# Kernel optimization log

Measured on AMD Instinct MI355X. Metric: run time of the kernel, lower is better.

Reference implementation:

```python
import jax, jax.numpy as jnp
import numpy as np

N_NODES = 50000

def gcn_conv(x, src, dst, W, b, n_nodes):
    # PyG GCNConv: add self-loops, symmetric deg^{-1/2} normalization,
    # linear transform, scatter-add aggregation (source -> target), bias.
    loop = jnp.arange(n_nodes, dtype=src.dtype)
    src2 = jnp.concatenate([src, loop])
    dst2 = jnp.concatenate([dst, loop])
    deg = jax.ops.segment_sum(jnp.ones_like(dst2, dtype=x.dtype), dst2, num_segments=n_nodes)
    dinv = jnp.where(deg > 0, jax.lax.rsqrt(deg), 0.0)
    norm = dinv[src2] * dinv[dst2]  # [E + N]
    h = x @ W                        # [N, out]
    msg = h[src2] * norm[:, None]    # gather + scale
    out = jax.ops.segment_sum(msg, dst2, num_segments=n_nodes)
    return out + b

def setup_inputs() -> dict:
    key = jax.random.key(0)
    k1, k2, k3, k4 = jax.random.split(key, 4)
    x = jax.random.normal(k1, (N_NODES, 64), dtype=jnp.float32)
    edge_index = jax.random.randint(k2, (2, 800000), 0, N_NODES, dtype=jnp.int64)
    # Glorot-ish init for weights
    W1 = jax.random.normal(k3, (64, 128), dtype=jnp.float32) * (1.0 / np.sqrt(64))
    b1 = jnp.zeros((128,), dtype=jnp.float32)
    W2 = jax.random.normal(k4, (128, 8), dtype=jnp.float32) * (1.0 / np.sqrt(128))
    b2 = jnp.zeros((8,), dtype=jnp.float32)
    return {"x": x, "edge_index": edge_index, "W1": W1, "b1": b1, "W2": W2, "b2": b2}

def reference(x, edge_index, W1, b1, W2, b2):
    src, dst = edge_index[0], edge_index[1]
    h = gcn_conv(x, src, dst, W1, b1, N_NODES)
    h = jax.nn.relu(h)
    out = gcn_conv(h, src, dst, W2, b2, N_NODES)
    return out
```

## Files before the change

### kernel.cpp

```cpp
#include <hip/hip_runtime.h>

#define IN1 64
#define MID 128
#define OUT2 8
#define YPAD 136
#define CAP 64

__device__ __forceinline__ unsigned short f2bf(float f) {
    unsigned int u = __float_as_uint(f);
    unsigned int r = (u + 0x7fff + ((u >> 16) & 1)) >> 16;
    return (unsigned short)r;
}
__device__ __forceinline__ float bflo(unsigned int u) { return __uint_as_float(u << 16); }
__device__ __forceinline__ float bfhi(unsigned int u) { return __uint_as_float(u & 0xffff0000u); }

__global__ __launch_bounds__(256) void k_fillp(const int* __restrict__ src,
                                               const int* __restrict__ dst,
                                               int* __restrict__ cnt,
                                               unsigned short* __restrict__ col,
                                               int E4, int E, int npx, int slices) {
    int xcd = blockIdx.x & 7;
    int slice = blockIdx.x >> 3;
    int lo = xcd * npx, hi = lo + npx;
    int eps = (E4 + slices - 1) / slices;
    int g0 = slice * eps, g1 = min(E4, g0 + eps);
    for (int g = g0 + (int)threadIdx.x; g < g1; g += 256) {
        int4 sv = ((const int4*)src)[g];
        int4 dv = ((const int4*)dst)[g];
        if (dv.x >= lo && dv.x < hi) {
            int p = atomicAdd(&cnt[dv.x], 1);
            if (p < CAP) col[dv.x * CAP + p] = (unsigned short)sv.x;
        }
        if (dv.y >= lo && dv.y < hi) {
            int p = atomicAdd(&cnt[dv.y], 1);
            if (p < CAP) col[dv.y * CAP + p] = (unsigned short)sv.y;
        }
        if (dv.z >= lo && dv.z < hi) {
            int p = atomicAdd(&cnt[dv.z], 1);
            if (p < CAP) col[dv.z * CAP + p] = (unsigned short)sv.z;
        }
        if (dv.w >= lo && dv.w < hi) {
            int p = atomicAdd(&cnt[dv.w], 1);
            if (p < CAP) col[dv.w * CAP + p] = (unsigned short)sv.w;
        }
    }
    if (blockIdx.x == 0 && threadIdx.x == 0) {
        for (int e = E4 * 4; e < E; ++e) {
            int d = dst[e];
            int p = atomicAdd(&cnt[d], 1);
            if (p < CAP) col[d * CAP + p] = (unsigned short)src[e];
        }
    }
}

__global__ void k_prescale(const float4* __restrict__ x4, const int* __restrict__ cnt,
                           float* __restrict__ dinv, ushort4* __restrict__ xb4, int n16) {
    int gid = blockIdx.x * blockDim.x + threadIdx.x;
    if (gid >= n16) return;
    int row = gid >> 4;
    float d = rsqrtf((float)(cnt[row] + 1));
    if ((gid & 15) == 0) dinv[row] = d;
    float4 vx = x4[gid];
    ushort4 p;
    p.x = f2bf(vx.x * d); p.y = f2bf(vx.y * d);
    p.z = f2bf(vx.z * d); p.w = f2bf(vx.w * d);
    xb4[gid] = p;
}

__global__ __launch_bounds__(256) void k_node(const uint2* __restrict__ xb2,
                                              const int* __restrict__ cnt,
                                              const unsigned short* __restrict__ col,
                                              const float* __restrict__ dinv,
                                              const float* __restrict__ W1,
                                              const float* __restrict__ b1,
                                              const float* __restrict__ W2,
                                              float* __restrict__ z, int n) {
    __shared__ float w2s[MID * OUT2];
    __shared__ float tS[4][4][IN1];
    __shared__ float yS[4][4][YPAD];

    int t = threadIdx.x;
    ((float4*)w2s)[t] = ((const float4*)W2)[t];

    int lane = t & 63, wave = t >> 6;
    int g = lane >> 4;
    int fl2 = lane & 15;
    int q4 = fl2 & 3;
    int row0 = blockIdx.x * 16 + wave * 4;
    int row = row0 + g;
    bool valid = row < n;

    float a0 = 0.f, a1 = 0.f, a2 = 0.f, a3 = 0.f;
    int deg = 0, base = 0;
    if (valid) {
        deg = min(cnt[row], CAP);
        base = row * CAP;
        uint2 u = xb2[(size_t)row * 16 + fl2];
        a0 = bflo(u.x); a1 = bfhi(u.x); a2 = bflo(u.y); a3 = bfhi(u.y);
    }
    int j = 0;
    for (; j + 4 <= deg; j += 4) {
        int cv = col[base + j + q4];
#pragma unroll
        for (int p = 0; p < 4; ++p) {
            int s = __shfl(cv, (g << 4) + p, 64);
            uint2 u = xb2[(size_t)s * 16 + fl2];
            a0 += bflo(u.x); a1 += bfhi(u.x);
            a2 += bflo(u.y); a3 += bfhi(u.y);
        }
    }
    int rem = deg - j;
    if (rem > 0) {
        int cv = col[base + min(j + q4, CAP - 1)];
#pragma unroll
        for (int p = 0; p < 4; ++p) {
            int s = __shfl(cv, (g << 4) + p, 64);
            if (p < rem) {
                uint2 u = xb2[(size_t)s * 16 + fl2];
                a0 += bflo(u.x); a1 += bfhi(u.x);
                a2 += bflo(u.y); a3 += bfhi(u.y);
            }
        }
    }
    {
        float4 w = {a0, a1, a2, a3};
        *(float4*)&tS[wave][g][4 * fl2] = w;
    }

    float dnd[4];
#pragma unroll
    for (int k = 0; k < 4; ++k) dnd[k] = dinv[min(row0 + k, n - 1)];

    float ya0 = 0.f, yb0 = 0.f, ya1 = 0.f, yb1 = 0.f;
    float ya2 = 0.f, yb2 = 0.f, ya3 = 0.f, yb3 = 0.f;
#pragma unroll 4
    for (int k4 = 0; k4 < IN1; k4 += 4) {
        float4 t0 = *(const float4*)&tS[wave][0][k4];
        float4 t1 = *(const float4*)&tS[wave][1][k4];
        float4 t2 = *(const float4*)&tS[wave][2][k4];
        float4 t3 = *(const float4*)&tS[wave][3][k4];
#pragma unroll
        for (int kk = 0; kk < 4; ++kk) {
            int k = k4 + kk;
            float wa = W1[k * MID + lane];
            float wb = W1[k * MID + lane + 64];
            float e0 = (&t0.x)[kk], e1 = (&t1.x)[kk], e2 = (&t2.x)[kk], e3 = (&t3.x)[kk];
            ya0 = fmaf(e0, wa, ya0); yb0 = fmaf(e0, wb, yb0);
            ya1 = fmaf(e1, wa, ya1); yb1 = fmaf(e1, wb, yb1);
            ya2 = fmaf(e2, wa, ya2); yb2 = fmaf(e2, wb, yb2);
            ya3 = fmaf(e3, wa, ya3); yb3 = fmaf(e3, wb, yb3);
        }
    }
    float bl = b1[lane], bh = b1[lane + 64];
    yS[wave][0][lane] = fmaxf(fmaf(ya0, dnd[0], bl), 0.f);
    yS[wave][0][lane + 64] = fmaxf(fmaf(yb0, dnd[0], bh), 0.f);
    yS[wave][1][lane] = fmaxf(fmaf(ya1, dnd[1], bl), 0.f);
    yS[wave][1][lane + 64] = fmaxf(fmaf(yb1, dnd[1], bh), 0.f);
    yS[wave][2][lane] = fmaxf(fmaf(ya2, dnd[2], bl), 0.f);
    yS[wave][2][lane + 64] = fmaxf(fmaf(yb2, dnd[2], bh), 0.f);
    yS[wave][3][lane] = fmaxf(fmaf(ya3, dnd[3], bl), 0.f);
    yS[wave][3][lane + 64] = fmaxf(fmaf(yb3, dnd[3], bh), 0.f);

    __syncthreads();

    int nd2 = lane >> 4, ch = lane & 15;
    float p[OUT2];
#pragma unroll
    for (int c = 0; c < OUT2; ++c) p[c] = 0.0f;
#pragma unroll
    for (int kk = 0; kk < 8; ++kk) {
        int k = kk * 16 + ch;
        float yk = yS[wave][nd2][k];
        float4 wlo = *(const float4*)&w2s[k * OUT2];
        float4 whi = *(const float4*)&w2s[k * OUT2 + 4];
        p[0] = fmaf(yk, wlo.x, p[0]); p[1] = fmaf(yk, wlo.y, p[1]);
        p[2] = fmaf(yk, wlo.z, p[2]); p[3] = fmaf(yk, wlo.w, p[3]);
        p[4] = fmaf(yk, whi.x, p[4]); p[5] = fmaf(yk, whi.y, p[5]);
        p[6] = fmaf(yk, whi.z, p[6]); p[7] = fmaf(yk, whi.w, p[7]);
    }
#pragma unroll
    for (int off = 1; off < 16; off <<= 1) {
#pragma unroll
        for (int c = 0; c < OUT2; ++c) p[c] += __shfl_xor(p[c], off, 64);
    }
    int rw = row0 + nd2;
    if (rw < n && ch < OUT2) {
        z[(size_t)rw * OUT2 + ch] = p[ch] * dinv[rw];
    }
}

__global__ __launch_bounds__(256) void k_gather2(const int* __restrict__ cnt,
                                                 const unsigned short* __restrict__ col,
                                                 const float* __restrict__ z,
                                                 const float* __restrict__ dinv,
                                                 const float* __restrict__ b2,
                                                 float* __restrict__ out, int n) {
    int t = threadIdx.x, lane = t & 63, wave = t >> 6;
    int node = blockIdx.x * 4 + wave;
    if (node >= n) return;
    int nb = lane >> 3, c = lane & 7;
    float acc = (nb == 0) ? z[(size_t)node * OUT2 + c] : 0.0f;
    int deg = min(cnt[node], CAP);
    int base = node * CAP;
    int j = nb;
    for (; j + 8 < deg; j += 16) {
        int s0 = col[base + j], s1 = col[base + j + 8];
        float a0 = z[(size_t)s0 * OUT2 + c];
        float a1 = z[(size_t)s1 * OUT2 + c];
        acc += a0 + a1;
    }
    if (j < deg) acc += z[(size_t)col[base + j] * OUT2 + c];
#pragma unroll
    for (int off = 8; off < 64; off <<= 1) acc += __shfl_xor(acc, off, 64);
    if (lane < OUT2) out[(size_t)node * OUT2 + lane] = fmaf(acc, dinv[node], b2[lane]);
}

extern "C" void kernel_launch(void* const* d_in, const int* in_sizes, int n_in,
                              void* d_out, int out_size, void* d_ws, size_t ws_size,
                              hipStream_t stream) {
    const float* x  = (const float*)d_in[0];
    const int*   ei = (const int*)d_in[1];
    const float* W1 = (const float*)d_in[2];
    const float* b1 = (const float*)d_in[3];
    const float* W2 = (const float*)d_in[4];
    const float* b2 = (const float*)d_in[5];
    float* out = (float*)d_out;

    int N = in_sizes[0] / IN1;
    int E = in_sizes[1] / 2;
    const int* src = ei;
    const int* dst = ei + E;

    int* cnt = (int*)d_ws;
    unsigned short* col = (unsigned short*)(cnt + N);
    float* dinv = (float*)(col + (size_t)N * CAP);
    float* z = dinv + N;
    unsigned short* xb = (unsigned short*)(z + (size_t)N * OUT2);

    const int B = 256;
    int E4 = E / 4;
    int npx = (N + 7) / 8;
    int slices = 192;

    hipMemsetAsync(cnt, 0, (size_t)N * sizeof(int), stream);
    k_fillp<<<slices * 8, B, 0, stream>>>(src, dst, cnt, col, E4, E, npx, slices);
    k_prescale<<<((size_t)N * 16 + B - 1) / B, B, 0, stream>>>((const float4*)x, cnt, dinv,
                                                               (ushort4*)xb, N * 16);
    k_node<<<(N + 15) / 16, 256, 0, stream>>>((const uint2*)xb, cnt, col, dinv, W1, b1, W2, z, N);
    k_gather2<<<(N + 3) / 4, 256, 0, stream>>>(cnt, col, z, dinv, b2, out, N);
}
```

Measured before the change: 169.4 us.

## Process eight rows per wave in node kernel with 16-byte gathers

The node kernel now handles 8 destination rows per wave instead of 4. Each lane gathers a full 16-byte chunk (8 bf16 features) per neighbor, which halves the number of gather instructions, and each W1 load is reused across twice as many rows in the dense transform. The fill kernel now reads src as scalars only when an edge falls in the block's range, instead of loading it as int4 for every edge. The trade-offs are higher register pressure from 16 accumulators, fewer blocks in the node kernel, and scattered scalar src loads.

```diff
diff --git a/kernel.cpp b/kernel.cpp
--- a/kernel.cpp
+++ b/kernel.cpp
@@ -4,6 +4,7 @@
 #define MID 128
 #define OUT2 8
 #define YPAD 136
+#define TPAD 68
 #define CAP 64
 
 __device__ __forceinline__ unsigned short f2bf(float f) {
@@ -25,23 +26,22 @@
     int eps = (E4 + slices - 1) / slices;
     int g0 = slice * eps, g1 = min(E4, g0 + eps);
     for (int g = g0 + (int)threadIdx.x; g < g1; g += 256) {
-        int4 sv = ((const int4*)src)[g];
         int4 dv = ((const int4*)dst)[g];
         if (dv.x >= lo && dv.x < hi) {
             int p = atomicAdd(&cnt[dv.x], 1);
-            if (p < CAP) col[dv.x * CAP + p] = (unsigned short)sv.x;
+            if (p < CAP) col[dv.x * CAP + p] = (unsigned short)src[4 * g];
         }
         if (dv.y >= lo && dv.y < hi) {
             int p = atomicAdd(&cnt[dv.y], 1);
-            if (p < CAP) col[dv.y * CAP + p] = (unsigned short)sv.y;
+            if (p < CAP) col[dv.y * CAP + p] = (unsigned short)src[4 * g + 1];
         }
         if (dv.z >= lo && dv.z < hi) {
             int p = atomicAdd(&cnt[dv.z], 1);
-            if (p < CAP) col[dv.z * CAP + p] = (unsigned short)sv.z;
+            if (p < CAP) col[dv.z * CAP + p] = (unsigned short)src[4 * g + 2];
         }
         if (dv.w >= lo && dv.w < hi) {
             int p = atomicAdd(&cnt[dv.w], 1);
-            if (p < CAP) col[dv.w * CAP + p] = (unsigned short)sv.w;
+            if (p < CAP) col[dv.w * CAP + p] = (unsigned short)src[4 * g + 3];
         }
     }
     if (blockIdx.x == 0 && threadIdx.x == 0) {
@@ -67,7 +67,7 @@
     xb4[gid] = p;
 }
 
-__global__ __launch_bounds__(256) void k_node(const uint2* __restrict__ xb2,
+__global__ __launch_bounds__(256) void k_node(const uint4* __restrict__ xb4,
                                               const int* __restrict__ cnt,
                                               const unsigned short* __restrict__ col,
                                               const float* __restrict__ dinv,
@@ -76,100 +76,100 @@
                                               const float* __restrict__ W2,
                                               float* __restrict__ z, int n) {
     __shared__ float w2s[MID * OUT2];
-    __shared__ float tS[4][4][IN1];
-    __shared__ float yS[4][4][YPAD];
+    __shared__ float tS[4][8][TPAD];
+    __shared__ float yS[4][8][YPAD];
 
     int t = threadIdx.x;
     ((float4*)w2s)[t] = ((const float4*)W2)[t];
 
     int lane = t & 63, wave = t >> 6;
-    int g = lane >> 4;
-    int fl2 = lane & 15;
-    int q4 = fl2 & 3;
-    int row0 = blockIdx.x * 16 + wave * 4;
+    int g = lane >> 3;
+    int fl = lane & 7;
+    int row0 = blockIdx.x * 32 + wave * 8;
     int row = row0 + g;
     bool valid = row < n;
 
-    float a0 = 0.f, a1 = 0.f, a2 = 0.f, a3 = 0.f;
+    float a0=0.f,a1=0.f,a2=0.f,a3=0.f,a4=0.f,a5=0.f,a6=0.f,a7=0.f;
     int deg = 0, base = 0;
     if (valid) {
         deg = min(cnt[row], CAP);
         base = row * CAP;
-        uint2 u = xb2[(size_t)row * 16 + fl2];
+        uint4 u = xb4[(size_t)row * 8 + fl];
         a0 = bflo(u.x); a1 = bfhi(u.x); a2 = bflo(u.y); a3 = bfhi(u.y);
+        a4 = bflo(u.z); a5 = bfhi(u.z); a6 = bflo(u.w); a7 = bfhi(u.w);
     }
     int j = 0;
-    for (; j + 4 <= deg; j += 4) {
-        int cv = col[base + j + q4];
-#pragma unroll
-        for (int p = 0; p < 4; ++p) {
-            int s = __shfl(cv, (g << 4) + p, 64);
-            uint2 u = xb2[(size_t)s * 16 + fl2];
-            a0 += bflo(u.x); a1 += bfhi(u.x);
-            a2 += bflo(u.y); a3 += bfhi(u.y);
+    for (; j + 8 <= deg; j += 8) {
+        int cv = col[base + j + fl];
+#pragma unroll
+        for (int p = 0; p < 8; ++p) {
+            int s = __shfl(cv, (g << 3) + p, 64);
+            uint4 u = xb4[(size_t)s * 8 + fl];
+            a0 += bflo(u.x); a1 += bfhi(u.x); a2 += bflo(u.y); a3 += bfhi(u.y);
+            a4 += bflo(u.z); a5 += bfhi(u.z); a6 += bflo(u.w); a7 += bfhi(u.w);
         }
     }
     int rem = deg - j;
     if (rem > 0) {
-        int cv = col[base + min(j + q4, CAP - 1)];
-#pragma unroll
-        for (int p = 0; p < 4; ++p) {
-            int s = __shfl(cv, (g << 4) + p, 64);
+        int cv = col[base + min(j + fl, CAP - 1)];
+#pragma unroll
+        for (int p = 0; p < 8; ++p) {
             if (p < rem) {
-                uint2 u = xb2[(size_t)s * 16 + fl2];
-                a0 += bflo(u.x); a1 += bfhi(u.x);
-                a2 += bflo(u.y); a3 += bfhi(u.y);
+                int s = __shfl(cv, (g << 3) + p, 64);
+                uint4 u = xb4[(size_t)s * 8 + fl];
+                a0 += bflo(u.x); a1 += bfhi(u.x); a2 += bflo(u.y); a3 += bfhi(u.y);
+                a4 += bflo(u.z); a5 += bfhi(u.z); a6 += bflo(u.w); a7 += bfhi(u.w);
             }
         }
     }
     {
-        float4 w = {a0, a1, a2, a3};
-        *(float4*)&tS[wave][g][4 * fl2] = w;
-    }
-
-    float dnd[4];
-#pragma unroll
-    for (int k = 0; k < 4; ++k) dnd[k] = dinv[min(row0 + k, n - 1)];
-
-    float ya0 = 0.f, yb0 = 0.f, ya1 = 0.f, yb1 = 0.f;
-    float ya2 = 0.f, yb2 = 0.f, ya3 = 0.f, yb3 = 0.f;
-#pragma unroll 4
+        float4 w0 = {a0, a1, a2, a3};
+        float4 w1v = {a4, a5, a6, a7};
+        *(float4*)&tS[wave][g][8 * fl] = w0;
+        *(float4*)&tS[wave][g][8 * fl + 4] = w1v;
+    }
+
+    float dnd[8];
+#pragma unroll
+    for (int k = 0; k < 8; ++k) dnd[k] = dinv[min(row0 + k, n - 1)];
+
+    float ya[8], yb[8];
+#pragma unroll
+    for (int i = 0; i < 8; ++i) { ya[i] = 0.f; yb[i] = 0.f; }
+#pragma unroll 2
     for (int k4 = 0; k4 < IN1; k4 += 4) {
-        float4 t0 = *(const float4*)&tS[wave][0][k4];
-        float4 t1 = *(const float4*)&tS[wave][1][k4];
-        float4 t2 = *(const float4*)&tS[wave][2][k4];
-        float4 t3 = *(const float4*)&tS[wave][3][k4];
+        float4 tv[8];
+#pragma unroll
+        for (int nd = 0; nd < 8; ++nd) tv[nd] = *(const float4*)&tS[wave][nd][k4];
 #pragma unroll
         for (int kk = 0; kk < 4; ++kk) {
             int k = k4 + kk;
             float wa = W1[k * MID + lane];
             float wb = W1[k * MID + lane + 64];
-            float e0 = (&t0.x)[kk], e1 = (&t1.x)[kk], e2 = (&t2.x)[kk], e3 = (&t3.x)[kk];
-            ya0 = fmaf(e0, wa, ya0); yb0 = fmaf(e0, wb, yb0);
-            ya1 = fmaf(e1, wa, ya1); yb1 = fmaf(e1, wb, yb1);
-            ya2 = fmaf(e2, wa, ya2); yb2 = fmaf(e2, wb, yb2);
-            ya3 = fmaf(e3, wa, ya3); yb3 = fmaf(e3, wb, yb3);
+#pragma unroll
+            for (int nd = 0; nd < 8; ++nd) {
+                float e = (&tv[nd].x)[kk];
+                ya[nd] = fmaf(e, wa, ya[nd]);
+                yb[nd] = fmaf(e, wb, yb[nd]);
+            }
         }
     }
     float bl = b1[lane], bh = b1[lane + 64];
-    yS[wave][0][lane] = fmaxf(fmaf(ya0, dnd[0], bl), 0.f);
-    yS[wave][0][lane + 64] = fmaxf(fmaf(yb0, dnd[0], bh), 0.f);
-    yS[wave][1][lane] = fmaxf(fmaf(ya1, dnd[1], bl), 0.f);
-    yS[wave][1][lane + 64] = fmaxf(fmaf(yb1, dnd[1], bh), 0.f);
-    yS[wave][2][lane] = fmaxf(fmaf(ya2, dnd[2], bl), 0.f);
-    yS[wave][2][lane + 64] = fmaxf(fmaf(yb2, dnd[2], bh), 0.f);
-    yS[wave][3][lane] = fmaxf(fmaf(ya3, dnd[3], bl), 0.f);
-    yS[wave][3][lane + 64] = fmaxf(fmaf(yb3, dnd[3], bh), 0.f);
+#pragma unroll
+    for (int nd = 0; nd < 8; ++nd) {
+        yS[wave][nd][lane] = fmaxf(fmaf(ya[nd], dnd[nd], bl), 0.f);
+        yS[wave][nd][lane + 64] = fmaxf(fmaf(yb[nd], dnd[nd], bh), 0.f);
+    }
 
     __syncthreads();
 
-    int nd2 = lane >> 4, ch = lane & 15;
+    int nd2 = lane >> 3, ch = lane & 7;
     float p[OUT2];
 #pragma unroll
     for (int c = 0; c < OUT2; ++c) p[c] = 0.0f;
 #pragma unroll
-    for (int kk = 0; kk < 8; ++kk) {
-        int k = kk * 16 + ch;
+    for (int kk = 0; kk < 16; ++kk) {
+        int k = kk * 8 + ch;
         float yk = yS[wave][nd2][k];
         float4 wlo = *(const float4*)&w2s[k * OUT2];
         float4 whi = *(const float4*)&w2s[k * OUT2 + 4];
@@ -179,12 +179,12 @@
         p[6] = fmaf(yk, whi.z, p[6]); p[7] = fmaf(yk, whi.w, p[7]);
     }
 #pragma unroll
-    for (int off = 1; off < 16; off <<= 1) {
+    for (int off = 1; off < 8; off <<= 1) {
 #pragma unroll
         for (int c = 0; c < OUT2; ++c) p[c] += __shfl_xor(p[c], off, 64);
     }
     int rw = row0 + nd2;
-    if (rw < n && ch < OUT2) {
+    if (rw < n) {
         z[(size_t)rw * OUT2 + ch] = p[ch] * dinv[rw];
     }
 }
@@ -246,6 +246,6 @@
     k_fillp<<<slices * 8, B, 0, stream>>>(src, dst, cnt, col, E4, E, npx, slices);
     k_prescale<<<((size_t)N * 16 + B - 1) / B, B, 0, stream>>>((const float4*)x, cnt, dinv,
                                                                (ushort4*)xb, N * 16);
-    k_node<<<(N + 15) / 16, 256, 0, stream>>>((const uint2*)xb, cnt, col, dinv, W1, b1, W2, z, N);
+    k_node<<<(N + 31) / 32, 256, 0, stream>>>((const uint4*)xb, cnt, col, dinv, W1, b1, W2, z, N);
     k_gather2<<<(N + 3) / 4, 256, 0, stream>>>(cnt, col, z, dinv, b2, out, N);
 }
```

Measured after the change: 165.8 us. -2.1%, faster.
